# Optimization experiments

Measured on AMD Instinct MI355X. Metric: run time of the kernel, lower is better.

The kernel has to match this reference:

```python
import jax, jax.numpy as jnp
import numpy as np

B, N, E = 2, 10000, 160000
D, DC, L = 512, 8, 3
EPS = 1e-5


def layer_norm(x, g, b):
    m = jnp.mean(x, axis=-1, keepdims=True)
    v = jnp.mean((x - m) ** 2, axis=-1, keepdims=True)
    return (x - m) * jax.lax.rsqrt(v + EPS) * g + b


def setup_inputs() -> dict:
    key = jax.random.key(0)
    ks = jax.random.split(key, 8)
    node_features = jax.random.normal(ks[0], (B, N, D), dtype=jnp.float32)
    edge_index = jax.random.randint(ks[1], (2, E), 0, N, dtype=jnp.int64)
    edge_attr = jax.random.normal(ks[2], (E, D), dtype=jnp.float32)
    # manifold coordinate projection
    W_coord = jax.random.normal(ks[3], (D, DC), dtype=jnp.float32) / np.sqrt(D)
    # per-layer causal field layers (modeled as linear) and layer norms
    W_field = jax.random.normal(ks[4], (L, D, D), dtype=jnp.float32) / np.sqrt(D)
    b_field = jnp.zeros((L, D), dtype=jnp.float32)
    ln_g = jnp.ones((L, D), dtype=jnp.float32)
    ln_b = jnp.zeros((L, D), dtype=jnp.float32)
    # output projection: LayerNorm + Linear
    out_ln_g = jnp.ones((D,), dtype=jnp.float32)
    out_ln_b = jnp.zeros((D,), dtype=jnp.float32)
    W_out = jax.random.normal(ks[5], (D, D), dtype=jnp.float32) / np.sqrt(D)
    b_out = jnp.zeros((D,), dtype=jnp.float32)
    return dict(node_features=node_features, edge_index=edge_index, edge_attr=edge_attr,
                W_coord=W_coord, W_field=W_field, b_field=b_field, ln_g=ln_g, ln_b=ln_b,
                out_ln_g=out_ln_g, out_ln_b=out_ln_b, W_out=W_out, b_out=b_out)


def reference(node_features, edge_index, edge_attr, W_coord, W_field, b_field,
              ln_g, ln_b, out_ln_g, out_ln_b, W_out, b_out):
    src, dst = edge_index[0], edge_index[1]
    # node coordinates from manifold projection (computed once, from inputs)
    coords = node_features @ W_coord                        # (B, N, DC)
    # transport factor per edge, per batch: exp(-||dst_coord - src_coord||)
    coord_diff = coords[:, dst] - coords[:, src]            # (B, E, DC)
    transport = jnp.exp(-jnp.linalg.norm(coord_diff, axis=-1, keepdims=True))  # (B, E, 1)
    # degree of destination nodes (same for every batch element)
    deg = jnp.zeros((N,), dtype=node_features.dtype).at[dst].add(1.0)
    deg = jnp.clip(deg, 1.0, None)[None, :, None]           # (1, N, 1)

    x = node_features
    edge_msg = None
    for l in range(L):
        x_field = x @ W_field[l] + b_field[l]               # (B, N, D)
        # gather src features, apply transport, add edge attributes
        edge_msg = x_field[:, src] * transport + edge_attr[None]  # (B, E, D)
        # scatter-add into destination nodes, normalize by degree
        upd = jnp.zeros_like(x).at[:, dst].add(edge_msg)    # (B, N, D)
        x = layer_norm(x + upd / deg, ln_g[l], ln_b[l])
    node_output = layer_norm(x, out_ln_g, out_ln_b) @ W_out + b_out
    return node_output, edge_msg
```

## Files before the change

kernel.cpp:

```cpp
#include <hip/hip_runtime.h>
#include <stdint.h>

#define NN 10000
#define EE 160000
#define BB 2
#define DD 512
#define KC 1024
#define MVALID 20000
#define MPAD 20096
#define LEPS 1e-5f

typedef __bf16 bf16_t;
typedef __bf16 bf16x8 __attribute__((ext_vector_type(8)));
typedef float f32x4 __attribute__((ext_vector_type(4)));
typedef float f32x2 __attribute__((ext_vector_type(2)));

__device__ inline void gload16(const void* g, void* l) {
  __builtin_amdgcn_global_load_lds((const __attribute__((address_space(1))) uint32_t*)g,
                                   (__attribute__((address_space(3))) uint32_t*)l,
                                   16, 0, 0);
}

__global__ __launch_bounds__(256) void convw_k(const float* __restrict__ Wf,
                                               const float* __restrict__ Wo,
                                               const float* __restrict__ olng,
                                               bf16_t* __restrict__ wcat) {
  __shared__ float tile[64][65];
  const int kt = blockIdx.x, nt = blockIdx.y, l = blockIdx.z;
  const float* W = (l < 3) ? (Wf + (size_t)l * 262144) : Wo;
  const int tn = threadIdx.x & 63;
  const int tk = threadIdx.x >> 6;
#pragma unroll
  for (int i = 0; i < 16; i++) {
    const int kl = tk + i * 4;
    tile[kl][tn] = W[(size_t)(kt * 64 + kl) * 512 + nt * 64 + tn];
  }
  __syncthreads();
  const int kl2 = threadIdx.x & 63;
  const int nb = threadIdx.x >> 6;
  const float gk = (l == 3) ? olng[kt * 64 + kl2] : 1.0f;
#pragma unroll
  for (int i = 0; i < 16; i++) {
    const int nl = nb + i * 4;
    bf16_t h = (bf16_t)(tile[kl2][nl] * gk);
    wcat[((size_t)l * 512 + nt * 64 + nl) * 512 + kt * 64 + kl2] = h;
  }
}

__global__ __launch_bounds__(512) void ubinit_k(const float* __restrict__ bo, float* __restrict__ ub) {
  ub[threadIdx.x] = bo[threadIdx.x];
}
__global__ __launch_bounds__(256) void ubacc_k(const float* __restrict__ olnb,
                                               const float* __restrict__ Wo,
                                               float* __restrict__ ub) {
  const int k0 = blockIdx.x * 16;
  const int tid = threadIdx.x;
#pragma unroll
  for (int h = 0; h < 2; h++) {
    const int n = tid + h * 256;
    float s = 0.f;
#pragma unroll
    for (int kk = 0; kk < 16; kk++) s += olnb[k0 + kk] * Wo[(size_t)(k0 + kk) * 512 + n];
    atomicAdd(&ub[n], s);
  }
}

__global__ __launch_bounds__(256) void coords_k(const float* __restrict__ x,
                                                const float* __restrict__ Wc,
                                                float* __restrict__ out,
                                                bf16_t* __restrict__ xcat) {
  __shared__ float smW[DD * 8];
  for (int i = threadIdx.x; i < DD * 8; i += 256) smW[i] = Wc[i];
  __syncthreads();
  const int wave = threadIdx.x >> 6, lane = threadIdx.x & 63;
  const int n = blockIdx.x * 4 + wave;
  const int b = blockIdx.y;
  const size_t row = (size_t)b * NN + n;
  const float* xr = x + row * DD + lane * 8;
  f32x4 x0 = *(const f32x4*)xr;
  f32x4 x1 = *(const f32x4*)(xr + 4);
  bf16x8 hi, lo;
#pragma unroll
  for (int j = 0; j < 8; j++) {
    float v = (j < 4) ? x0[j] : x1[j - 4];
    bf16_t h = (bf16_t)v;
    hi[j] = h;
    lo[j] = (bf16_t)(v - (float)h);
  }
  bf16_t* xc = xcat + row * KC + lane * 8;
  *(bf16x8*)xc = hi;
  *(bf16x8*)(xc + DD) = lo;
  float a[8];
#pragma unroll
  for (int dc = 0; dc < 8; dc++) a[dc] = 0.f;
#pragma unroll
  for (int j = 0; j < 8; j++) {
    float xv = (j < 4) ? x0[j] : x1[j - 4];
    const float* wrow = smW + (lane * 8 + j) * 8;
#pragma unroll
    for (int dc = 0; dc < 8; dc++) a[dc] += xv * wrow[dc];
  }
#pragma unroll
  for (int dc = 0; dc < 8; dc++)
    for (int o = 32; o >= 1; o >>= 1) a[dc] += __shfl_xor(a[dc], o);
  if (lane == 0) {
#pragma unroll
    for (int dc = 0; dc < 8; dc++) out[row * 8 + dc] = a[dc];
  }
}

__global__ __launch_bounds__(256) void transport_deg_k(const float* __restrict__ coords,
                                                       const int* __restrict__ srcA,
                                                       const int* __restrict__ dstA,
                                                       float* __restrict__ tr,
                                                       int* __restrict__ degc) {
  int e = blockIdx.x * 256 + threadIdx.x;
  int s = srcA[e], d = dstA[e];
#pragma unroll
  for (int b = 0; b < BB; b++) {
    const float* cs = coords + ((size_t)b * NN + s) * 8;
    const float* cd = coords + ((size_t)b * NN + d) * 8;
    float ss = 0.f;
#pragma unroll
    for (int i = 0; i < 8; i++) {
      float df = cd[i] - cs[i];
      ss += df * df;
    }
    tr[(size_t)b * EE + e] = expf(-sqrtf(ss));
  }
  atomicAdd(&degc[d], 1);
}

__global__ __launch_bounds__(1024) void scan_k(const int* __restrict__ cnt, int* __restrict__ rowptr,
                                               float* __restrict__ invdeg) {
  __shared__ int part[1024];
  const int tid = threadIdx.x;
  const int CH = 10;
  int base = tid * CH;
  int local[CH];
  int s = 0;
#pragma unroll
  for (int i = 0; i < CH; i++) {
    int n = base + i;
    int c = (n < NN) ? cnt[n] : 0;
    local[i] = s;
    s += c;
  }
  part[tid] = s;
  __syncthreads();
  for (int off = 1; off < 1024; off <<= 1) {
    int v = (tid >= off) ? part[tid - off] : 0;
    __syncthreads();
    part[tid] += v;
    __syncthreads();
  }
  int excl = (tid > 0) ? part[tid - 1] : 0;
#pragma unroll
  for (int i = 0; i < CH; i++) {
    int n = base + i;
    if (n < NN) {
      rowptr[n] = excl + local[i];
      int c = cnt[n];
      invdeg[n] = 1.0f / (float)(c > 1 ? c : 1);
    }
  }
  if (tid == 0) rowptr[NN] = EE;
}

__global__ __launch_bounds__(256) void fillremap_k(const int* __restrict__ srcA,
                                                   const int* __restrict__ dstA,
                                                   const int* __restrict__ rowptr,
                                                   const float* __restrict__ tr,
                                                   const float* __restrict__ invdeg,
                                                   int* __restrict__ fill,
                                                   int* __restrict__ eidA,
                                                   int* __restrict__ srcs,
                                                   float* __restrict__ trs) {
  int e = blockIdx.x * 256 + threadIdx.x;
  const int d = dstA[e];
  const int pos = rowptr[d] + atomicAdd(&fill[d], 1);
  const float idg = invdeg[d];
  eidA[pos] = e;
  srcs[pos] = srcA[e];
  trs[pos] = tr[e] * idg;
  trs[(size_t)EE + pos] = tr[(size_t)EE + e] * idg;
}

__global__ __launch_bounds__(256) void gemm_bt_b(const bf16_t* __restrict__ A,
                                                 const bf16_t* __restrict__ Bw,
                                                 const float* __restrict__ bias,
                                                 bf16_t* __restrict__ C, int mvalid) {
  __shared__ __align__(16) char smem[16384];
  const int tid = threadIdx.x;
  const int lane = tid & 63;
  const int wave = tid >> 6;
  const int mtile = blockIdx.x;
  const int ntile = blockIdx.y;
  const int wr = wave >> 1, wc = wave & 1;
  const int r = tid >> 2;
  const int c = tid & 3;
  const size_t aRow0 = (size_t)(mtile * 128 + r);
  const size_t bRow0 = (size_t)(ntile * 128 + r);
  char* smA = smem;
  char* smB = smem + 8192;
  char* ldsA0 = smA + tid * 16;
  char* ldsA1 = smA + 4096 + tid * 16;
  char* ldsB0 = smB + tid * 16;
  char* ldsB1 = smB + 4096 + tid * 16;

  f32x4 acc[4][4];
#pragma unroll
  for (int m = 0; m < 4; m++)
#pragma unroll
    for (int n = 0; n < 4; n++) acc[m][n] = (f32x4){0.f, 0.f, 0.f, 0.f};

  const int koff = (lane >> 4) * 16;
  const int arow = wr * 64 + (lane & 15);
  const int brow = wc * 64 + (lane & 15);

  for (int kk = 0; kk < 16; ++kk) {
    const int kbase = kk * 32 + c * 8;
    gload16(A + aRow0 * KC + kbase, ldsA0);
    gload16(A + (aRow0 + 64) * KC + kbase, ldsA1);
    gload16(Bw + bRow0 * 512 + kbase, ldsB0);
    gload16(Bw + (bRow0 + 64) * 512 + kbase, ldsB1);
    __syncthreads();
    bf16x8 af[4], bfr[4];
#pragma unroll
    for (int m = 0; m < 4; m++) af[m] = *(const bf16x8*)(smA + (arow + m * 16) * 64 + koff);
#pragma unroll
    for (int n = 0; n < 4; n++) bfr[n] = *(const bf16x8*)(smB + (brow + n * 16) * 64 + koff);
#pragma unroll
    for (int m = 0; m < 4; m++)
#pragma unroll
      for (int n = 0; n < 4; n++)
        acc[m][n] = __builtin_amdgcn_mfma_f32_16x16x32_bf16(af[m], bfr[n], acc[m][n], 0, 0, 0);
    __syncthreads();
  }

  const int crow0 = mtile * 128 + wr * 64 + (lane >> 4) * 4;
  const int ccol0 = ntile * 128 + wc * 64 + (lane & 15);
#pragma unroll
  for (int n = 0; n < 4; n++) {
    const int col = ccol0 + n * 16;
    const float bv = bias[col];
#pragma unroll
    for (int m = 0; m < 4; m++) {
      const int rw = crow0 + m * 16;
#pragma unroll
      for (int j = 0; j < 4; j++) {
        int rowi = rw + j;
        if (rowi < mvalid) C[(size_t)rowi * DD + col] = (bf16_t)(acc[m][n][j] + bv);
      }
    }
  }
}

__global__ __launch_bounds__(256) void gemm_bt_f(const bf16_t* __restrict__ A,
                                                 const bf16_t* __restrict__ Bw,
                                                 const float* __restrict__ bias,
                                                 float* __restrict__ C, int mvalid,
                                                 const float* __restrict__ rs) {
  __shared__ __align__(16) char smem[16384];
  const int tid = threadIdx.x;
  const int lane = tid & 63;
  const int wave = tid >> 6;
  const int mtile = blockIdx.x;
  const int ntile = blockIdx.y;
  const int wr = wave >> 1, wc = wave & 1;
  const int r = tid >> 2;
  const int c = tid & 3;
  const size_t aRow0 = (size_t)(mtile * 128 + r);
  const size_t bRow0 = (size_t)(ntile * 128 + r);
  char* smA = smem;
  char* smB = smem + 8192;
  char* ldsA0 = smA + tid * 16;
  char* ldsA1 = smA + 4096 + tid * 16;
  char* ldsB0 = smB + tid * 16;
  char* ldsB1 = smB + 4096 + tid * 16;

  f32x4 acc[4][4];
#pragma unroll
  for (int m = 0; m < 4; m++)
#pragma unroll
    for (int n = 0; n < 4; n++) acc[m][n] = (f32x4){0.f, 0.f, 0.f, 0.f};

  const int koff = (lane >> 4) * 16;
  const int arow = wr * 64 + (lane & 15);
  const int brow = wc * 64 + (lane & 15);

  for (int kk = 0; kk < 16; ++kk) {
    const int kbase = kk * 32 + c * 8;
    gload16(A + aRow0 * KC + kbase, ldsA0);
    gload16(A + (aRow0 + 64) * KC + kbase, ldsA1);
    gload16(Bw + bRow0 * 512 + kbase, ldsB0);
    gload16(Bw + (bRow0 + 64) * 512 + kbase, ldsB1);
    __syncthreads();
    bf16x8 af[4], bfr[4];
#pragma unroll
    for (int m = 0; m < 4; m++) af[m] = *(const bf16x8*)(smA + (arow + m * 16) * 64 + koff);
#pragma unroll
    for (int n = 0; n < 4; n++) bfr[n] = *(const bf16x8*)(smB + (brow + n * 16) * 64 + koff);
#pragma unroll
    for (int m = 0; m < 4; m++)
#pragma unroll
      for (int n = 0; n < 4; n++)
        acc[m][n] = __builtin_amdgcn_mfma_f32_16x16x32_bf16(af[m], bfr[n], acc[m][n], 0, 0, 0);
    __syncthreads();
  }

  const int crow0 = mtile * 128 + wr * 64 + (lane >> 4) * 4;
  const int ccol0 = ntile * 128 + wc * 64 + (lane & 15);
#pragma unroll
  for (int n = 0; n < 4; n++) {
    const int col = ccol0 + n * 16;
    const float bv = bias[col];
#pragma unroll
    for (int m = 0; m < 4; m++) {
      const int rw = crow0 + m * 16;
#pragma unroll
      for (int j = 0; j < 4; j++) {
        int rowi = rw + j;
        if (rowi < mvalid) C[(size_t)rowi * DD + col] = acc[m][n][j] * rs[rowi] + bv;
      }
    }
  }
}

template <int FUSE_EA>
__device__ inline void layer_body(int n, int lane,
                                  const bf16_t* __restrict__ xfield, int outstat,
                                  bf16_t* __restrict__ xcat,
                                  const int* __restrict__ srcs,
                                  const float* __restrict__ trs,
                                  const int* __restrict__ rowptr,
                                  const int* __restrict__ eidA,
                                  const float* __restrict__ eattr,
                                  const float* __restrict__ invdeg,
                                  float* __restrict__ eagg,
                                  const float* __restrict__ g,
                                  const float* __restrict__ bbias,
                                  float* __restrict__ rs_out) {
  const int d0 = lane * 8;
  const int beg = rowptr[n], end = rowptr[n + 1];
  const bf16_t* xf0 = xfield + (size_t)0 * NN * DD + d0;
  const bf16_t* xf1 = xfield + (size_t)1 * NN * DD + d0;
  const float* trs1p = trs + EE;
  float acc0[8], acc1[8], eac[8];
#pragma unroll
  for (int j = 0; j < 8; j++) acc0[j] = acc1[j] = eac[j] = 0.f;

  for (int c0 = beg; c0 < end; c0 += 64) {
    const int cnt = min(64, end - c0);
    int s_r = 0, e_r = 0;
    float t0_r = 0.f, t1_r = 0.f;
    if (lane < cnt) {
      s_r = srcs[c0 + lane];
      t0_r = trs[c0 + lane];
      t1_r = trs1p[c0 + lane];
      if (FUSE_EA) e_r = eidA[c0 + lane];
    }
    for (int j = 0; j < cnt; j += 4) {
#pragma unroll
      for (int u = 0; u < 4; u++) {
        const int jj = j + u;
        const int s = __shfl(s_r, jj);
        const float t0 = __shfl(t0_r, jj);
        const float t1 = __shfl(t1_r, jj);
        const bf16x8 xv0 = *(const bf16x8*)(xf0 + (size_t)s * DD);
        const bf16x8 xv1 = *(const bf16x8*)(xf1 + (size_t)s * DD);
        if (FUSE_EA) {
          const int e = __shfl(e_r, jj);
          const bool act = jj < cnt;
          const f32x4 r0 = __builtin_nontemporal_load((const f32x4*)(eattr + (size_t)e * DD + d0));
          const f32x4 r1 = __builtin_nontemporal_load((const f32x4*)(eattr + (size_t)e * DD + d0 + 4));
          if (act) {
#pragma unroll
            for (int q = 0; q < 8; q++) eac[q] += (q < 4) ? r0[q & 3] : r1[q & 3];
          }
        }
#pragma unroll
        for (int q = 0; q < 8; q++) {
          acc0[q] += t0 * (float)xv0[q];
          acc1[q] += t1 * (float)xv1[q];
        }
      }
    }
  }

  float ea8[8];
  if (FUSE_EA) {
    const float idg = invdeg[n];
#pragma unroll
    for (int j = 0; j < 8; j++) ea8[j] = eac[j] * idg;
    f32x4 o0, o1;
#pragma unroll
    for (int j = 0; j < 4; j++) {
      o0[j] = ea8[j];
      o1[j] = ea8[j + 4];
    }
    *(f32x4*)(eagg + (size_t)n * DD + d0) = o0;
    *(f32x4*)(eagg + (size_t)n * DD + d0 + 4) = o1;
  } else {
    const f32x4 e0 = *(const f32x4*)(eagg + (size_t)n * DD + d0);
    const f32x4 e1 = *(const f32x4*)(eagg + (size_t)n * DD + d0 + 4);
#pragma unroll
    for (int j = 0; j < 8; j++) ea8[j] = (j < 4) ? e0[j] : e1[j - 4];
  }

  bf16_t* xc0 = xcat + (size_t)n * KC + d0;
  bf16_t* xc1 = xcat + (size_t)(NN + n) * KC + d0;
  const bf16x8 h0 = *(const bf16x8*)(xc0);
  const bf16x8 l0v = *(const bf16x8*)(xc0 + DD);
  const bf16x8 h1 = *(const bf16x8*)(xc1);
  const bf16x8 l1v = *(const bf16x8*)(xc1 + DD);
  float v0[8], v1[8];
  float s10 = 0.f, s20 = 0.f, s11 = 0.f, s21 = 0.f;
#pragma unroll
  for (int j = 0; j < 8; j++) {
    const float xp0 = (float)h0[j] + (float)l0v[j];
    const float xp1 = (float)h1[j] + (float)l1v[j];
    v0[j] = xp0 + acc0[j] + ea8[j];
    v1[j] = xp1 + acc1[j] + ea8[j];
    s10 += v0[j];
    s20 += v0[j] * v0[j];
    s11 += v1[j];
    s21 += v1[j] * v1[j];
  }
#pragma unroll
  for (int o = 32; o >= 1; o >>= 1) {
    s10 += __shfl_xor(s10, o);
    s20 += __shfl_xor(s20, o);
    s11 += __shfl_xor(s11, o);
    s21 += __shfl_xor(s21, o);
  }
  const float mean0 = s10 * (1.f / 512.f);
  const float rs0 = rsqrtf(s20 * (1.f / 512.f) - mean0 * mean0 + LEPS);
  const float mean1 = s11 * (1.f / 512.f);
  const float rs1 = rsqrtf(s21 * (1.f / 512.f) - mean1 * mean1 + LEPS);
  const f32x4 g0 = *(const f32x4*)(g + d0);
  const f32x4 g1 = *(const f32x4*)(g + d0 + 4);
  const f32x4 b0 = *(const f32x4*)(bbias + d0);
  const f32x4 b1 = *(const f32x4*)(bbias + d0 + 4);
  float y0[8], y1[8];
  float sy10 = 0.f, sy20 = 0.f, sy11 = 0.f, sy21 = 0.f;
#pragma unroll
  for (int j = 0; j < 8; j++) {
    const float gg = (j < 4) ? g0[j] : g1[j - 4];
    const float bb = (j < 4) ? b0[j] : b1[j - 4];
    y0[j] = (v0[j] - mean0) * rs0 * gg + bb;
    y1[j] = (v1[j] - mean1) * rs1 * gg + bb;
    sy10 += y0[j];
    sy20 += y0[j] * y0[j];
    sy11 += y1[j];
    sy21 += y1[j] * y1[j];
  }
  float sub0 = 0.f, sub1 = 0.f;
  if (outstat) {
#pragma unroll
    for (int o = 32; o >= 1; o >>= 1) {
      sy10 += __shfl_xor(sy10, o);
      sy20 += __shfl_xor(sy20, o);
      sy11 += __shfl_xor(sy11, o);
      sy21 += __shfl_xor(sy21, o);
    }
    const float my0 = sy10 * (1.f / 512.f);
    const float rsy0 = rsqrtf(sy20 * (1.f / 512.f) - my0 * my0 + LEPS);
    const float my1 = sy11 * (1.f / 512.f);
    const float rsy1 = rsqrtf(sy21 * (1.f / 512.f) - my1 * my1 + LEPS);
    if (lane == 0) {
      rs_out[n] = rsy0;
      rs_out[NN + n] = rsy1;
    }
    sub0 = my0;
    sub1 = my1;
  }
  bf16x8 ho0, lo0, ho1, lo1;
#pragma unroll
  for (int j = 0; j < 8; j++) {
    const float ya = y0[j] - sub0;
    const float yb = y1[j] - sub1;
    bf16_t ha = (bf16_t)ya;
    bf16_t hb = (bf16_t)yb;
    ho0[j] = ha;
    lo0[j] = (bf16_t)(ya - (float)ha);
    ho1[j] = hb;
    lo1[j] = (bf16_t)(yb - (float)hb);
  }
  *(bf16x8*)xc0 = ho0;
  *(bf16x8*)xc1 = ho1;
  if (!outstat) {
    *(bf16x8*)(xc0 + DD) = lo0;
    *(bf16x8*)(xc1 + DD) = lo1;
  }
}

template <int FUSE_EA>
__global__ __launch_bounds__(256) void layer_k(const bf16_t* __restrict__ xfield,
                                               bf16_t* __restrict__ xcat,
                                               const int* __restrict__ srcs,
                                               const float* __restrict__ trs,
                                               const int* __restrict__ rowptr,
                                               const int* __restrict__ eidA,
                                               const float* __restrict__ eattr,
                                               const float* __restrict__ invdeg,
                                               float* __restrict__ eagg,
                                               const float* __restrict__ g,
                                               const float* __restrict__ bbias) {
  const int wave = threadIdx.x >> 6, lane = threadIdx.x & 63;
  const int n = blockIdx.x * 4 + wave;
  layer_body<FUSE_EA>(n, lane, xfield, 0, xcat, srcs, trs, rowptr, eidA, eattr, invdeg, eagg, g,
                      bbias, nullptr);
}

__global__ __launch_bounds__(256) void tail_k(const bf16_t* __restrict__ xfield,
                                              bf16_t* __restrict__ xcat,
                                              const int* __restrict__ srcs,
                                              const float* __restrict__ trs,
                                              const int* __restrict__ rowptr,
                                              const float* __restrict__ eagg,
                                              const float* __restrict__ g,
                                              const float* __restrict__ bbias,
                                              float* __restrict__ rs_out,
                                              const float* __restrict__ transport,
                                              const int* __restrict__ srcA,
                                              const float* __restrict__ eattr,
                                              float* __restrict__ outE) {
  const int bid = blockIdx.x;
  const int wv = threadIdx.x >> 6, lane = threadIdx.x & 63;
  if (bid < 2500) {
    const int n = bid * 4 + wv;
    layer_body<0>(n, lane, xfield, 1, xcat, srcs, trs, rowptr, nullptr, nullptr, nullptr,
                  (float*)eagg, g, bbias, rs_out);
  } else {
    const int e = (bid - 2500) * 4 + wv;
    const int d0 = lane * 8;
    const int s = srcA[e];
    const f32x4 a0 = __builtin_nontemporal_load((const f32x4*)(eattr + (size_t)e * DD + d0));
    const f32x4 a1 = __builtin_nontemporal_load((const f32x4*)(eattr + (size_t)e * DD + d0 + 4));
    const float t0 = transport[e];
    const float t1 = transport[(size_t)EE + e];
    const bf16x8 x0 = *(const bf16x8*)(xfield + (size_t)s * DD + d0);
    const bf16x8 x1 = *(const bf16x8*)(xfield + ((size_t)NN + s) * DD + d0);
    f32x4 o00, o01, o10, o11;
#pragma unroll
    for (int j = 0; j < 4; j++) {
      o00[j] = (float)x0[j] * t0 + a0[j];
      o01[j] = (float)x0[j + 4] * t0 + a1[j];
      o10[j] = (float)x1[j] * t1 + a0[j];
      o11[j] = (float)x1[j + 4] * t1 + a1[j];
    }
    float* ob0 = outE + (size_t)e * DD + d0;
    float* ob1 = outE + ((size_t)EE + e) * DD + d0;
    __builtin_nontemporal_store(o00, (f32x4*)ob0);
    __builtin_nontemporal_store(o01, (f32x4*)(ob0 + 4));
    __builtin_nontemporal_store(o10, (f32x4*)ob1);
    __builtin_nontemporal_store(o11, (f32x4*)(ob1 + 4));
  }
}

extern "C" void kernel_launch(void* const* d_in, const int* in_sizes, int n_in,
                              void* d_out, int out_size, void* d_ws, size_t ws_size,
                              hipStream_t stream) {
  const float* nf = (const float*)d_in[0];
  const int* eidx = (const int*)d_in[1];
  const float* eattr = (const float*)d_in[2];
  const float* Wc = (const float*)d_in[3];
  const float* Wf = (const float*)d_in[4];
  const float* bfield = (const float*)d_in[5];
  const float* lng = (const float*)d_in[6];
  const float* lnb = (const float*)d_in[7];
  const float* olng = (const float*)d_in[8];
  const float* olnb = (const float*)d_in[9];
  const float* Wo = (const float*)d_in[10];
  const float* bo = (const float*)d_in[11];
  const int* srcA = eidx;
  const int* dstA = eidx + EE;
  float* outp = (float*)d_out;

  char* ws = (char*)d_ws;
  size_t off = 0;
  auto alloc = [&](size_t bytes) {
    void* p = ws + off;
    off += (bytes + 255) & ~(size_t)255;
    return p;
  };
  bf16_t* xcat = (bf16_t*)alloc((size_t)MPAD * KC * 2);
  bf16_t* xfield = (bf16_t*)alloc((size_t)MPAD * DD * 2);
  bf16_t* wcat = (bf16_t*)alloc((size_t)4 * DD * 512 * 2);
  float* eagg = (float*)alloc((size_t)NN * DD * 4);
  float* coords = (float*)alloc((size_t)BB * NN * 8 * 4);
  float* transport = (float*)alloc((size_t)BB * EE * 4);
  float* trs = (float*)alloc((size_t)BB * EE * 4);
  int* srcs = (int*)alloc(EE * 4);
  int* degfill = (int*)alloc((size_t)2 * NN * 4);
  int* degc = degfill;
  int* fillb = degfill + NN;
  int* rowptr = (int*)alloc((NN + 1) * 4);
  int* eidl = (int*)alloc(EE * 4);
  float* invdeg = (float*)alloc(NN * 4);
  float* rs_out = (float*)alloc((size_t)BB * NN * 4);
  float* ub = (float*)alloc(DD * 4);

  hipMemsetAsync(degfill, 0, (size_t)2 * NN * 4, stream);
  hipMemsetAsync(xcat + (size_t)MVALID * KC, 0, (size_t)(MPAD - MVALID) * KC * 2, stream);

  convw_k<<<dim3(8, 8, 4), 256, 0, stream>>>(Wf, Wo, olng, wcat);
  ubinit_k<<<1, 512, 0, stream>>>(bo, ub);
  ubacc_k<<<32, 256, 0, stream>>>(olnb, Wo, ub);
  coords_k<<<dim3(2500, 2), 256, 0, stream>>>(nf, Wc, coords, xcat);
  transport_deg_k<<<625, 256, 0, stream>>>(coords, srcA, dstA, transport, degc);
  scan_k<<<1, 1024, 0, stream>>>(degc, rowptr, invdeg);
  fillremap_k<<<625, 256, 0, stream>>>(srcA, dstA, rowptr, transport, invdeg, fillb, eidl, srcs,
                                       trs);

  for (int l = 0; l < 2; l++) {
    gemm_bt_b<<<dim3(157, 4), 256, 0, stream>>>(xcat, wcat + (size_t)l * DD * 512,
                                                bfield + l * DD, xfield, MVALID);
    if (l == 0)
      layer_k<1><<<2500, 256, 0, stream>>>(xfield, xcat, srcs, trs, rowptr, eidl, eattr, invdeg,
                                           eagg, lng + l * DD, lnb + l * DD);
    else
      layer_k<0><<<2500, 256, 0, stream>>>(xfield, xcat, srcs, trs, rowptr, eidl, eattr, invdeg,
                                           eagg, lng + l * DD, lnb + l * DD);
  }
  gemm_bt_b<<<dim3(157, 4), 256, 0, stream>>>(xcat, wcat + (size_t)2 * DD * 512, bfield + 2 * DD,
                                              xfield, MVALID);
  tail_k<<<42500, 256, 0, stream>>>(xfield, xcat, srcs, trs, rowptr, eagg, lng + 2 * DD,
                                    lnb + 2 * DD, rs_out, transport, srcA, eattr,
                                    outp + (size_t)BB * NN * DD);
  gemm_bt_f<<<dim3(157, 4), 256, 0, stream>>>(xcat, wcat + (size_t)3 * DD * 512, ub, outp, MVALID,
                                              rs_out);
}
```

Measured before the change: 644.8 us.

## Merge prologue kernels and co-schedule independent work into shared launches

The weight conversion, output-bias fold and coordinate/bf16 split kernels are merged into one prologue launch. The first field GEMM now shares a launch with the transport/degree computation, and the final output GEMM shares a launch with the edge-message output writes, with the last layer's node pass split out. This cuts launch count and lets independent work fill the GPU concurrently, at the cost of heterogeneous blocks in one grid, more LDS per block in the prologue, and the last node layer no longer overlapping the edge output.

```diff
diff --git a/kernel.cpp b/kernel.cpp
--- a/kernel.cpp
+++ b/kernel.cpp
@@ -13,7 +13,6 @@
 typedef __bf16 bf16_t;
 typedef __bf16 bf16x8 __attribute__((ext_vector_type(8)));
 typedef float f32x4 __attribute__((ext_vector_type(4)));
-typedef float f32x2 __attribute__((ext_vector_type(2)));
 
 __device__ inline void gload16(const void* g, void* l) {
   __builtin_amdgcn_global_load_lds((const __attribute__((address_space(1))) uint32_t*)g,
@@ -21,181 +20,15 @@
                                    16, 0, 0);
 }
 
-__global__ __launch_bounds__(256) void convw_k(const float* __restrict__ Wf,
-                                               const float* __restrict__ Wo,
-                                               const float* __restrict__ olng,
-                                               bf16_t* __restrict__ wcat) {
-  __shared__ float tile[64][65];
-  const int kt = blockIdx.x, nt = blockIdx.y, l = blockIdx.z;
-  const float* W = (l < 3) ? (Wf + (size_t)l * 262144) : Wo;
-  const int tn = threadIdx.x & 63;
-  const int tk = threadIdx.x >> 6;
-#pragma unroll
-  for (int i = 0; i < 16; i++) {
-    const int kl = tk + i * 4;
-    tile[kl][tn] = W[(size_t)(kt * 64 + kl) * 512 + nt * 64 + tn];
-  }
-  __syncthreads();
-  const int kl2 = threadIdx.x & 63;
-  const int nb = threadIdx.x >> 6;
-  const float gk = (l == 3) ? olng[kt * 64 + kl2] : 1.0f;
-#pragma unroll
-  for (int i = 0; i < 16; i++) {
-    const int nl = nb + i * 4;
-    bf16_t h = (bf16_t)(tile[kl2][nl] * gk);
-    wcat[((size_t)l * 512 + nt * 64 + nl) * 512 + kt * 64 + kl2] = h;
-  }
-}
-
-__global__ __launch_bounds__(512) void ubinit_k(const float* __restrict__ bo, float* __restrict__ ub) {
-  ub[threadIdx.x] = bo[threadIdx.x];
-}
-__global__ __launch_bounds__(256) void ubacc_k(const float* __restrict__ olnb,
-                                               const float* __restrict__ Wo,
-                                               float* __restrict__ ub) {
-  const int k0 = blockIdx.x * 16;
-  const int tid = threadIdx.x;
-#pragma unroll
-  for (int h = 0; h < 2; h++) {
-    const int n = tid + h * 256;
-    float s = 0.f;
-#pragma unroll
-    for (int kk = 0; kk < 16; kk++) s += olnb[k0 + kk] * Wo[(size_t)(k0 + kk) * 512 + n];
-    atomicAdd(&ub[n], s);
-  }
-}
-
-__global__ __launch_bounds__(256) void coords_k(const float* __restrict__ x,
-                                                const float* __restrict__ Wc,
-                                                float* __restrict__ out,
-                                                bf16_t* __restrict__ xcat) {
-  __shared__ float smW[DD * 8];
-  for (int i = threadIdx.x; i < DD * 8; i += 256) smW[i] = Wc[i];
-  __syncthreads();
-  const int wave = threadIdx.x >> 6, lane = threadIdx.x & 63;
-  const int n = blockIdx.x * 4 + wave;
-  const int b = blockIdx.y;
-  const size_t row = (size_t)b * NN + n;
-  const float* xr = x + row * DD + lane * 8;
-  f32x4 x0 = *(const f32x4*)xr;
-  f32x4 x1 = *(const f32x4*)(xr + 4);
-  bf16x8 hi, lo;
-#pragma unroll
-  for (int j = 0; j < 8; j++) {
-    float v = (j < 4) ? x0[j] : x1[j - 4];
-    bf16_t h = (bf16_t)v;
-    hi[j] = h;
-    lo[j] = (bf16_t)(v - (float)h);
-  }
-  bf16_t* xc = xcat + row * KC + lane * 8;
-  *(bf16x8*)xc = hi;
-  *(bf16x8*)(xc + DD) = lo;
-  float a[8];
-#pragma unroll
-  for (int dc = 0; dc < 8; dc++) a[dc] = 0.f;
-#pragma unroll
-  for (int j = 0; j < 8; j++) {
-    float xv = (j < 4) ? x0[j] : x1[j - 4];
-    const float* wrow = smW + (lane * 8 + j) * 8;
-#pragma unroll
-    for (int dc = 0; dc < 8; dc++) a[dc] += xv * wrow[dc];
-  }
-#pragma unroll
-  for (int dc = 0; dc < 8; dc++)
-    for (int o = 32; o >= 1; o >>= 1) a[dc] += __shfl_xor(a[dc], o);
-  if (lane == 0) {
-#pragma unroll
-    for (int dc = 0; dc < 8; dc++) out[row * 8 + dc] = a[dc];
-  }
-}
-
-__global__ __launch_bounds__(256) void transport_deg_k(const float* __restrict__ coords,
-                                                       const int* __restrict__ srcA,
-                                                       const int* __restrict__ dstA,
-                                                       float* __restrict__ tr,
-                                                       int* __restrict__ degc) {
-  int e = blockIdx.x * 256 + threadIdx.x;
-  int s = srcA[e], d = dstA[e];
-#pragma unroll
-  for (int b = 0; b < BB; b++) {
-    const float* cs = coords + ((size_t)b * NN + s) * 8;
-    const float* cd = coords + ((size_t)b * NN + d) * 8;
-    float ss = 0.f;
-#pragma unroll
-    for (int i = 0; i < 8; i++) {
-      float df = cd[i] - cs[i];
-      ss += df * df;
-    }
-    tr[(size_t)b * EE + e] = expf(-sqrtf(ss));
-  }
-  atomicAdd(&degc[d], 1);
-}
-
-__global__ __launch_bounds__(1024) void scan_k(const int* __restrict__ cnt, int* __restrict__ rowptr,
-                                               float* __restrict__ invdeg) {
-  __shared__ int part[1024];
-  const int tid = threadIdx.x;
-  const int CH = 10;
-  int base = tid * CH;
-  int local[CH];
-  int s = 0;
-#pragma unroll
-  for (int i = 0; i < CH; i++) {
-    int n = base + i;
-    int c = (n < NN) ? cnt[n] : 0;
-    local[i] = s;
-    s += c;
-  }
-  part[tid] = s;
-  __syncthreads();
-  for (int off = 1; off < 1024; off <<= 1) {
-    int v = (tid >= off) ? part[tid - off] : 0;
-    __syncthreads();
-    part[tid] += v;
-    __syncthreads();
-  }
-  int excl = (tid > 0) ? part[tid - 1] : 0;
-#pragma unroll
-  for (int i = 0; i < CH; i++) {
-    int n = base + i;
-    if (n < NN) {
-      rowptr[n] = excl + local[i];
-      int c = cnt[n];
-      invdeg[n] = 1.0f / (float)(c > 1 ? c : 1);
-    }
-  }
-  if (tid == 0) rowptr[NN] = EE;
-}
-
-__global__ __launch_bounds__(256) void fillremap_k(const int* __restrict__ srcA,
-                                                   const int* __restrict__ dstA,
-                                                   const int* __restrict__ rowptr,
-                                                   const float* __restrict__ tr,
-                                                   const float* __restrict__ invdeg,
-                                                   int* __restrict__ fill,
-                                                   int* __restrict__ eidA,
-                                                   int* __restrict__ srcs,
-                                                   float* __restrict__ trs) {
-  int e = blockIdx.x * 256 + threadIdx.x;
-  const int d = dstA[e];
-  const int pos = rowptr[d] + atomicAdd(&fill[d], 1);
-  const float idg = invdeg[d];
-  eidA[pos] = e;
-  srcs[pos] = srcA[e];
-  trs[pos] = tr[e] * idg;
-  trs[(size_t)EE + pos] = tr[(size_t)EE + e] * idg;
-}
-
-__global__ __launch_bounds__(256) void gemm_bt_b(const bf16_t* __restrict__ A,
-                                                 const bf16_t* __restrict__ Bw,
-                                                 const float* __restrict__ bias,
-                                                 bf16_t* __restrict__ C, int mvalid) {
-  __shared__ __align__(16) char smem[16384];
+
+template <int MODE>
+__device__ inline void gemm_body(char* smem, int mtile, int ntile,
+                                 const bf16_t* __restrict__ A, const bf16_t* __restrict__ Bw,
+                                 const float* __restrict__ bias, void* __restrict__ Cv,
+                                 const float* __restrict__ rs) {
   const int tid = threadIdx.x;
   const int lane = tid & 63;
   const int wave = tid >> 6;
-  const int mtile = blockIdx.x;
-  const int ntile = blockIdx.y;
   const int wr = wave >> 1, wc = wave & 1;
   const int r = tid >> 2;
   const int c = tid & 3;
@@ -250,78 +83,12 @@
 #pragma unroll
       for (int j = 0; j < 4; j++) {
         int rowi = rw + j;
-        if (rowi < mvalid) C[(size_t)rowi * DD + col] = (bf16_t)(acc[m][n][j] + bv);
-      }
-    }
-  }
-}
-
-__global__ __launch_bounds__(256) void gemm_bt_f(const bf16_t* __restrict__ A,
-                                                 const bf16_t* __restrict__ Bw,
-                                                 const float* __restrict__ bias,
-                                                 float* __restrict__ C, int mvalid,
-                                                 const float* __restrict__ rs) {
-  __shared__ __align__(16) char smem[16384];
-  const int tid = threadIdx.x;
-  const int lane = tid & 63;
-  const int wave = tid >> 6;
-  const int mtile = blockIdx.x;
-  const int ntile = blockIdx.y;
-  const int wr = wave >> 1, wc = wave & 1;
-  const int r = tid >> 2;
-  const int c = tid & 3;
-  const size_t aRow0 = (size_t)(mtile * 128 + r);
-  const size_t bRow0 = (size_t)(ntile * 128 + r);
-  char* smA = smem;
-  char* smB = smem + 8192;
-  char* ldsA0 = smA + tid * 16;
-  char* ldsA1 = smA + 4096 + tid * 16;
-  char* ldsB0 = smB + tid * 16;
-  char* ldsB1 = smB + 4096 + tid * 16;
-
-  f32x4 acc[4][4];
-#pragma unroll
-  for (int m = 0; m < 4; m++)
-#pragma unroll
-    for (int n = 0; n < 4; n++) acc[m][n] = (f32x4){0.f, 0.f, 0.f, 0.f};
-
-  const int koff = (lane >> 4) * 16;
-  const int arow = wr * 64 + (lane & 15);
-  const int brow = wc * 64 + (lane & 15);
-
-  for (int kk = 0; kk < 16; ++kk) {
-    const int kbase = kk * 32 + c * 8;
-    gload16(A + aRow0 * KC + kbase, ldsA0);
-    gload16(A + (aRow0 + 64) * KC + kbase, ldsA1);
-    gload16(Bw + bRow0 * 512 + kbase, ldsB0);
-    gload16(Bw + (bRow0 + 64) * 512 + kbase, ldsB1);
-    __syncthreads();
-    bf16x8 af[4], bfr[4];
-#pragma unroll
-    for (int m = 0; m < 4; m++) af[m] = *(const bf16x8*)(smA + (arow + m * 16) * 64 + koff);
-#pragma unroll
-    for (int n = 0; n < 4; n++) bfr[n] = *(const bf16x8*)(smB + (brow + n * 16) * 64 + koff);
-#pragma unroll
-    for (int m = 0; m < 4; m++)
-#pragma unroll
-      for (int n = 0; n < 4; n++)
-        acc[m][n] = __builtin_amdgcn_mfma_f32_16x16x32_bf16(af[m], bfr[n], acc[m][n], 0, 0, 0);
-    __syncthreads();
-  }
-
-  const int crow0 = mtile * 128 + wr * 64 + (lane >> 4) * 4;
-  const int ccol0 = ntile * 128 + wc * 64 + (lane & 15);
-#pragma unroll
-  for (int n = 0; n < 4; n++) {
-    const int col = ccol0 + n * 16;
-    const float bv = bias[col];
-#pragma unroll
-    for (int m = 0; m < 4; m++) {
-      const int rw = crow0 + m * 16;
-#pragma unroll
-      for (int j = 0; j < 4; j++) {
-        int rowi = rw + j;
-        if (rowi < mvalid) C[(size_t)rowi * DD + col] = acc[m][n][j] * rs[rowi] + bv;
+        if (rowi < MVALID) {
+          if constexpr (MODE == 0)
+            ((bf16_t*)Cv)[(size_t)rowi * DD + col] = (bf16_t)(acc[m][n][j] + bv);
+          else
+            ((float*)Cv)[(size_t)rowi * DD + col] = acc[m][n][j] * rs[rowi] + bv;
+        }
       }
     }
   }
@@ -495,6 +262,190 @@
   }
 }
 
+
+__global__ __launch_bounds__(256) void prologue_k(const float* __restrict__ Wf,
+                                                  const float* __restrict__ Wo,
+                                                  const float* __restrict__ olng,
+                                                  bf16_t* __restrict__ wcat,
+                                                  const float* __restrict__ olnb,
+                                                  const float* __restrict__ bo,
+                                                  float* __restrict__ ub,
+                                                  const float* __restrict__ x,
+                                                  const float* __restrict__ Wc,
+                                                  float* __restrict__ coords,
+                                                  bf16_t* __restrict__ xcat) {
+  __shared__ __align__(16) char shmem[16896];
+  const int bid = blockIdx.x;
+  if (bid < 256) {
+    float(*tile)[65] = (float(*)[65])shmem;
+    const int kt = bid & 7, nt = (bid >> 3) & 7, l = bid >> 6;
+    const float* W = (l < 3) ? (Wf + (size_t)l * 262144) : Wo;
+    const int tn = threadIdx.x & 63;
+    const int tk = threadIdx.x >> 6;
+#pragma unroll
+    for (int i = 0; i < 16; i++) {
+      const int kl = tk + i * 4;
+      tile[kl][tn] = W[(size_t)(kt * 64 + kl) * 512 + nt * 64 + tn];
+    }
+    __syncthreads();
+    const int kl2 = threadIdx.x & 63;
+    const int nb = threadIdx.x >> 6;
+    const float gk = (l == 3) ? olng[kt * 64 + kl2] : 1.0f;
+#pragma unroll
+    for (int i = 0; i < 16; i++) {
+      const int nl = nb + i * 4;
+      bf16_t h = (bf16_t)(tile[kl2][nl] * gk);
+      wcat[((size_t)l * 512 + nt * 64 + nl) * 512 + kt * 64 + kl2] = h;
+    }
+  } else if (bid < 288) {
+    const int k0 = (bid - 256) * 16;
+    const int tid = threadIdx.x;
+#pragma unroll
+    for (int h = 0; h < 2; h++) {
+      const int n = tid + h * 256;
+      float s = (k0 == 0) ? bo[n] : 0.f;
+#pragma unroll
+      for (int kk = 0; kk < 16; kk++) s += olnb[k0 + kk] * Wo[(size_t)(k0 + kk) * 512 + n];
+      atomicAdd(&ub[n], s);
+    }
+  } else {
+    float* smW = (float*)shmem;
+    for (int i = threadIdx.x; i < DD * 8; i += 256) smW[i] = Wc[i];
+    __syncthreads();
+    const int v = bid - 288;
+    const int wave = threadIdx.x >> 6, lane = threadIdx.x & 63;
+    const int n = (v >> 1) * 4 + wave;
+    const int b = v & 1;
+    const size_t row = (size_t)b * NN + n;
+    const float* xr = x + row * DD + lane * 8;
+    f32x4 x0 = *(const f32x4*)xr;
+    f32x4 x1 = *(const f32x4*)(xr + 4);
+    bf16x8 hi, lo;
+#pragma unroll
+    for (int j = 0; j < 8; j++) {
+      float vv = (j < 4) ? x0[j] : x1[j - 4];
+      bf16_t h = (bf16_t)vv;
+      hi[j] = h;
+      lo[j] = (bf16_t)(vv - (float)h);
+    }
+    bf16_t* xc = xcat + row * KC + lane * 8;
+    *(bf16x8*)xc = hi;
+    *(bf16x8*)(xc + DD) = lo;
+    float a[8];
+#pragma unroll
+    for (int dc = 0; dc < 8; dc++) a[dc] = 0.f;
+#pragma unroll
+    for (int j = 0; j < 8; j++) {
+      float xv = (j < 4) ? x0[j] : x1[j - 4];
+      const float* wrow = smW + (lane * 8 + j) * 8;
+#pragma unroll
+      for (int dc = 0; dc < 8; dc++) a[dc] += xv * wrow[dc];
+    }
+#pragma unroll
+    for (int dc = 0; dc < 8; dc++)
+      for (int o = 32; o >= 1; o >>= 1) a[dc] += __shfl_xor(a[dc], o);
+    if (lane == 0) {
+#pragma unroll
+      for (int dc = 0; dc < 8; dc++) coords[row * 8 + dc] = a[dc];
+    }
+  }
+}
+
+__global__ __launch_bounds__(256) void g0t_k(const bf16_t* __restrict__ A,
+                                             const bf16_t* __restrict__ Bw,
+                                             const float* __restrict__ bias,
+                                             bf16_t* __restrict__ C,
+                                             const float* __restrict__ coords,
+                                             const int* __restrict__ srcA,
+                                             const int* __restrict__ dstA,
+                                             float* __restrict__ tr,
+                                             int* __restrict__ degc) {
+  __shared__ __align__(16) char smem[16384];
+  const int bid = blockIdx.x;
+  if (bid < 628) {
+    gemm_body<0>(smem, bid % 157, bid / 157, A, Bw, bias, C, nullptr);
+  } else {
+    int e = (bid - 628) * 256 + threadIdx.x;
+    int s = srcA[e], d = dstA[e];
+#pragma unroll
+    for (int b = 0; b < BB; b++) {
+      const float* cs = coords + ((size_t)b * NN + s) * 8;
+      const float* cd = coords + ((size_t)b * NN + d) * 8;
+      float ss = 0.f;
+#pragma unroll
+      for (int i = 0; i < 8; i++) {
+        float df = cd[i] - cs[i];
+        ss += df * df;
+      }
+      tr[(size_t)b * EE + e] = expf(-sqrtf(ss));
+    }
+    atomicAdd(&degc[d], 1);
+  }
+}
+
+__global__ __launch_bounds__(1024) void scan_k(const int* __restrict__ cnt, int* __restrict__ rowptr,
+                                               float* __restrict__ invdeg) {
+  __shared__ int part[1024];
+  const int tid = threadIdx.x;
+  const int CH = 10;
+  int base = tid * CH;
+  int local[CH];
+  int s = 0;
+#pragma unroll
+  for (int i = 0; i < CH; i++) {
+    int n = base + i;
+    int c = (n < NN) ? cnt[n] : 0;
+    local[i] = s;
+    s += c;
+  }
+  part[tid] = s;
+  __syncthreads();
+  for (int off = 1; off < 1024; off <<= 1) {
+    int v = (tid >= off) ? part[tid - off] : 0;
+    __syncthreads();
+    part[tid] += v;
+    __syncthreads();
+  }
+  int excl = (tid > 0) ? part[tid - 1] : 0;
+#pragma unroll
+  for (int i = 0; i < CH; i++) {
+    int n = base + i;
+    if (n < NN) {
+      rowptr[n] = excl + local[i];
+      int c = cnt[n];
+      invdeg[n] = 1.0f / (float)(c > 1 ? c : 1);
+    }
+  }
+  if (tid == 0) rowptr[NN] = EE;
+}
+
+__global__ __launch_bounds__(256) void fillremap_k(const int* __restrict__ srcA,
+                                                   const int* __restrict__ dstA,
+                                                   const int* __restrict__ rowptr,
+                                                   const float* __restrict__ tr,
+                                                   const float* __restrict__ invdeg,
+                                                   int* __restrict__ fill,
+                                                   int* __restrict__ eidA,
+                                                   int* __restrict__ srcs,
+                                                   float* __restrict__ trs) {
+  int e = blockIdx.x * 256 + threadIdx.x;
+  const int d = dstA[e];
+  const int pos = rowptr[d] + atomicAdd(&fill[d], 1);
+  const float idg = invdeg[d];
+  eidA[pos] = e;
+  srcs[pos] = srcA[e];
+  trs[pos] = tr[e] * idg;
+  trs[(size_t)EE + pos] = tr[(size_t)EE + e] * idg;
+}
+
+__global__ __launch_bounds__(256) void gemm_bt_b(const bf16_t* __restrict__ A,
+                                                 const bf16_t* __restrict__ Bw,
+                                                 const float* __restrict__ bias,
+                                                 bf16_t* __restrict__ C) {
+  __shared__ __align__(16) char smem[16384];
+  gemm_body<0>(smem, blockIdx.x, blockIdx.y, A, Bw, bias, C, nullptr);
+}
+
 template <int FUSE_EA>
 __global__ __launch_bounds__(256) void layer_k(const bf16_t* __restrict__ xfield,
                                                bf16_t* __restrict__ xcat,
@@ -513,27 +464,38 @@
                       bbias, nullptr);
 }
 
-__global__ __launch_bounds__(256) void tail_k(const bf16_t* __restrict__ xfield,
-                                              bf16_t* __restrict__ xcat,
-                                              const int* __restrict__ srcs,
-                                              const float* __restrict__ trs,
-                                              const int* __restrict__ rowptr,
-                                              const float* __restrict__ eagg,
-                                              const float* __restrict__ g,
-                                              const float* __restrict__ bbias,
-                                              float* __restrict__ rs_out,
-                                              const float* __restrict__ transport,
-                                              const int* __restrict__ srcA,
-                                              const float* __restrict__ eattr,
-                                              float* __restrict__ outE) {
+__global__ __launch_bounds__(256) void layer2_k(const bf16_t* __restrict__ xfield,
+                                                bf16_t* __restrict__ xcat,
+                                                const int* __restrict__ srcs,
+                                                const float* __restrict__ trs,
+                                                const int* __restrict__ rowptr,
+                                                const float* __restrict__ eagg,
+                                                const float* __restrict__ g,
+                                                const float* __restrict__ bbias,
+                                                float* __restrict__ rs_out) {
+  const int wave = threadIdx.x >> 6, lane = threadIdx.x & 63;
+  const int n = blockIdx.x * 4 + wave;
+  layer_body<0>(n, lane, xfield, 1, xcat, srcs, trs, rowptr, nullptr, nullptr, nullptr,
+                (float*)eagg, g, bbias, rs_out);
+}
+
+__global__ __launch_bounds__(256) void emf_k(const bf16_t* __restrict__ xcat,
+                                             const bf16_t* __restrict__ BwF,
+                                             const float* __restrict__ ub,
+                                             float* __restrict__ outN,
+                                             const float* __restrict__ rs_out,
+                                             const bf16_t* __restrict__ xfield,
+                                             const float* __restrict__ transport,
+                                             const int* __restrict__ srcA,
+                                             const float* __restrict__ eattr,
+                                             float* __restrict__ outE) {
+  __shared__ __align__(16) char smem[16384];
   const int bid = blockIdx.x;
-  const int wv = threadIdx.x >> 6, lane = threadIdx.x & 63;
-  if (bid < 2500) {
-    const int n = bid * 4 + wv;
-    layer_body<0>(n, lane, xfield, 1, xcat, srcs, trs, rowptr, nullptr, nullptr, nullptr,
-                  (float*)eagg, g, bbias, rs_out);
+  if (bid < 628) {
+    gemm_body<1>(smem, bid % 157, bid / 157, xcat, BwF, ub, outN, rs_out);
   } else {
-    const int e = (bid - 2500) * 4 + wv;
+    const int wv = threadIdx.x >> 6, lane = threadIdx.x & 63;
+    const int e = (bid - 628) * 4 + wv;
     const int d0 = lane * 8;
     const int s = srcA[e];
     const f32x4 a0 = __builtin_nontemporal_load((const f32x4*)(eattr + (size_t)e * DD + d0));
@@ -593,42 +555,33 @@
   float* transport = (float*)alloc((size_t)BB * EE * 4);
   float* trs = (float*)alloc((size_t)BB * EE * 4);
   int* srcs = (int*)alloc(EE * 4);
-  int* degfill = (int*)alloc((size_t)2 * NN * 4);
-  int* degc = degfill;
-  int* fillb = degfill + NN;
+  char* zblk = (char*)alloc((size_t)2 * NN * 4 + DD * 4);
+  int* degc = (int*)zblk;
+  int* fillb = degc + NN;
+  float* ub = (float*)(zblk + (size_t)2 * NN * 4);
   int* rowptr = (int*)alloc((NN + 1) * 4);
   int* eidl = (int*)alloc(EE * 4);
   float* invdeg = (float*)alloc(NN * 4);
   float* rs_out = (float*)alloc((size_t)BB * NN * 4);
-  float* ub = (float*)alloc(DD * 4);
-
-  hipMemsetAsync(degfill, 0, (size_t)2 * NN * 4, stream);
+
+  hipMemsetAsync(zblk, 0, (size_t)2 * NN * 4 + DD * 4, stream);
   hipMemsetAsync(xcat + (size_t)MVALID * KC, 0, (size_t)(MPAD - MVALID) * KC * 2, stream);
 
-  convw_k<<<dim3(8, 8, 4), 256, 0, stream>>>(Wf, Wo, olng, wcat);
-  ubinit_k<<<1, 512, 0, stream>>>(bo, ub);
-  ubacc_k<<<32, 256, 0, stream>>>(olnb, Wo, ub);
-  coords_k<<<dim3(2500, 2), 256, 0, stream>>>(nf, Wc, coords, xcat);
-  transport_deg_k<<<625, 256, 0, stream>>>(coords, srcA, dstA, transport, degc);
+  prologue_k<<<5288, 256, 0, stream>>>(Wf, Wo, olng, wcat, olnb, bo, ub, nf, Wc, coords, xcat);
+  g0t_k<<<1253, 256, 0, stream>>>(xcat, wcat, bfield, xfield, coords, srcA, dstA, transport, degc);
   scan_k<<<1, 1024, 0, stream>>>(degc, rowptr, invdeg);
   fillremap_k<<<625, 256, 0, stream>>>(srcA, dstA, rowptr, transport, invdeg, fillb, eidl, srcs,
                                        trs);
-
-  for (int l = 0; l < 2; l++) {
-    gemm_bt_b<<<dim3(157, 4), 256, 0, stream>>>(xcat, wcat + (size_t)l * DD * 512,
-                                                bfield + l * DD, xfield, MVALID);
-    if (l == 0)
-      layer_k<1><<<2500, 256, 0, stream>>>(xfield, xcat, srcs, trs, rowptr, eidl, eattr, invdeg,
-                                           eagg, lng + l * DD, lnb + l * DD);
-    else
-      layer_k<0><<<2500, 256, 0, stream>>>(xfield, xcat, srcs, trs, rowptr, eidl, eattr, invdeg,
-                                           eagg, lng + l * DD, lnb + l * DD);
-  }
+  layer_k<1><<<2500, 256, 0, stream>>>(xfield, xcat, srcs, trs, rowptr, eidl, eattr, invdeg, eagg,
+                                       lng, lnb);
+  gemm_bt_b<<<dim3(157, 4), 256, 0, stream>>>(xcat, wcat + (size_t)1 * DD * 512, bfield + DD,
+                                              xfield);
+  layer_k<0><<<2500, 256, 0, stream>>>(xfield, xcat, srcs, trs, rowptr, eidl, eattr, invdeg, eagg,
+                                       lng + DD, lnb + DD);
   gemm_bt_b<<<dim3(157, 4), 256, 0, stream>>>(xcat, wcat + (size_t)2 * DD * 512, bfield + 2 * DD,
-                                              xfield, MVALID);
-  tail_k<<<42500, 256, 0, stream>>>(xfield, xcat, srcs, trs, rowptr, eagg, lng + 2 * DD,
-                                    lnb + 2 * DD, rs_out, transport, srcA, eattr,
-                                    outp + (size_t)BB * NN * DD);
-  gemm_bt_f<<<dim3(157, 4), 256, 0, stream>>>(xcat, wcat + (size_t)3 * DD * 512, ub, outp, MVALID,
-                                              rs_out);
-}
+                                              xfield);
+  layer2_k<<<2500, 256, 0, stream>>>(xfield, xcat, srcs, trs, rowptr, eagg, lng + 2 * DD,
+                                     lnb + 2 * DD, rs_out);
+  emf_k<<<40628, 256, 0, stream>>>(xcat, wcat + (size_t)3 * DD * 512, ub, outp, rs_out, xfield,
+                                   transport, srcA, eattr, outp + (size_t)BB * NN * DD);
+}
```

New measurement: 683.4 us. 6.0% more time.
